# Kernel optimization log

Hardware: AMD Instinct MI355X
Metric: run time of the kernel (lower is better)

The kernel has to match this reference:

```python
import jax, jax.numpy as jnp
import numpy as np

B, N, L, E, D = 16, 16384, 192, 128, 128


def setup_inputs() -> dict:
    key = jax.random.key(0)
    ks = jax.random.split(key, 16)
    s = 0.05
    return {
        "x_L_flattened": jax.random.normal(ks[0], (B, N), jnp.float32),
        "x_y_mask_flattened": jax.random.randint(ks[1], (B, N), 0, 2).astype(jnp.float32),
        "y_mask_L_flattened": jnp.zeros((B, N), jnp.float32),
        "x_y_mark": jax.random.normal(ks[2], (B, L, 1), jnp.float32),
        "variable_indices_flattened": jax.random.randint(ks[3], (B, N), 0, E),
        "time_indices_flattened": jax.random.randint(ks[4], (B, N), 0, L),
        "N_OBSERVATIONS_MAX": N,
        # learned params (stored [in, out]; torch Linear uses x @ W.T + b)
        "W_obs": jax.random.normal(ks[5], (2, D), jnp.float32) * s,
        "b_obs": jnp.zeros((D,), jnp.float32),
        "W_time": jax.random.normal(ks[6], (1, D), jnp.float32) * s,
        "b_time": jnp.zeros((D,), jnp.float32),
        "var_hyperedge_w": jax.random.normal(ks[7], (E, D), jnp.float32),
        "W_q": jax.random.normal(ks[8], (D, D), jnp.float32) * s,
        "b_q": jnp.zeros((D,), jnp.float32),
        "W_k": jax.random.normal(ks[9], (D, D), jnp.float32) * s,
        "b_k": jnp.zeros((D,), jnp.float32),
        "W_v": jax.random.normal(ks[10], (D, D), jnp.float32) * s,
        "b_v": jnp.zeros((D,), jnp.float32),
        "threshold": jnp.float32(0.5),
        "merge_coef": jnp.float32(0.5),
    }


def reference(x_L_flattened, x_y_mask_flattened, y_mask_L_flattened, x_y_mark,
              variable_indices_flattened, time_indices_flattened, N_OBSERVATIONS_MAX,
              W_obs, b_obs, W_time, b_time, var_hyperedge_w,
              W_q, b_q, W_k, b_k, W_v, b_v, threshold, merge_coef):
    mask = x_y_mask_flattened  # [B, N]
    # node features: value + (1 - mask + y_mask) channel -> [B, N, 2]
    feats = jnp.stack([x_L_flattened, 1.0 - mask + y_mask_L_flattened], axis=-1)
    # temporal incidence: node n belongs to time-edge l iff time_idx[n] == l; [B, L, N]
    ti = (time_indices_flattened[:, None, :] == jnp.arange(L)[None, :, None]).astype(jnp.float32)
    ti = ti * mask[:, None, :]
    # variable incidence: node n belongs to var-edge e iff var_idx[n] == e; [B, E, N]
    vi = (jnp.arange(E)[None, :, None] == variable_indices_flattened[:, None, :]).astype(jnp.float32)
    vi = vi * mask[:, None, :]
    # encoders
    obs = jax.nn.relu(feats @ W_obs + b_obs) * mask[..., None]          # [B, N, D]
    temp_he = jnp.sin(x_y_mark @ W_time + b_time)                        # [B, L, D]
    var_he = jax.nn.relu(jnp.broadcast_to(var_hyperedge_w, (B, E, D)))   # [B, E, D]
    # IrregularityAwareAttention over variable hyperedges with incidence as aux
    q = var_he @ W_q + b_q
    k = var_he @ W_k + b_k
    v = var_he @ W_v + b_v
    att = jnp.einsum('bed,bfd->bef', q, k) / (D ** 0.5)                  # [B, E, E]
    att_aux = jnp.einsum('ben,bfn->bef', vi, vi) / (N_OBSERVATIONS_MAX ** 0.5)
    merge = (att > threshold) & (att_aux != 0)
    att = jnp.where(merge, (1.0 - merge_coef) * att + merge_coef * att_aux, att)
    attn = jax.nn.softmax(att, axis=-1)
    out = jnp.einsum('bef,bfd->bed', attn, v)                            # [B, E, D]
    return (obs, temp_he, out, ti, vi)
```

## Files before the change

kernel.cpp:

```cpp
#include <hip/hip_runtime.h>

#define Bb 16
#define Nn 16384
#define Ll 192
#define Ee 128
#define Dd 128


__global__ __launch_bounds__(256) void k_obs(
    const float* __restrict__ x, const float* __restrict__ mask,
    const float* __restrict__ ymask, const int* __restrict__ vidx,
    const int* __restrict__ tidx, const float* __restrict__ W_obs,
    const float* __restrict__ b_obs, float* __restrict__ obs,
    float* __restrict__ ti, float* __restrict__ vi, float* __restrict__ cnt)
{
    const int row  = (blockIdx.x << 2) + (threadIdx.x >> 6);
    const int lane = threadIdx.x & 63;
    const int b = row >> 14;
    const int n = row & (Nn - 1);

    const float m  = mask[row];
    const float xv = x[row];
    const float f1 = 1.0f - m + ymask[row];

    const int d = lane << 1;
    const float w00 = W_obs[d],      w01 = W_obs[d + 1];
    const float w10 = W_obs[Dd + d], w11 = W_obs[Dd + d + 1];
    const float bb0 = b_obs[d],      bb1 = b_obs[d + 1];

    float2 ov;
    ov.x = fmaxf(fmaf(xv, w00, fmaf(f1, w10, bb0)), 0.0f) * m;
    ov.y = fmaxf(fmaf(xv, w01, fmaf(f1, w11, bb1)), 0.0f) * m;
    *reinterpret_cast<float2*>(obs + ((size_t)row << 7) + d) = ov;

    if (lane == 0 && m != 0.0f) {
        const int t = tidx[row];
        const int e = vidx[row];
        ti[(size_t)b * (Ll * (size_t)Nn) + (size_t)t * Nn + n] = m;
        vi[((size_t)(b * Ee + e) << 14) + n] = m;
        atomicAdd(&cnt[b * Ee + e], 1.0f);
    }
}

__global__ __launch_bounds__(256) void k_temp(
    const float* __restrict__ mark, const float* __restrict__ Wt,
    const float* __restrict__ bt, float* __restrict__ temp)
{
    const int idx = blockIdx.x * 256 + threadIdx.x;
    const int d = idx & 127;
    const int r = idx >> 7;
    temp[idx] = sinf(fmaf(mark[r], Wt[d], bt[d]));
}

__global__ __launch_bounds__(128) void k_qkv(
    const float* __restrict__ var_w,
    const float* __restrict__ Wq, const float* __restrict__ bq,
    const float* __restrict__ Wk, const float* __restrict__ bk,
    const float* __restrict__ Wv, const float* __restrict__ bv,
    float* __restrict__ q, float* __restrict__ k, float* __restrict__ v)
{
    __shared__ float h[Dd];
    const int e = blockIdx.x, d = threadIdx.x;
    h[d] = fmaxf(var_w[e * Dd + d], 0.0f);
    __syncthreads();
    float aq = bq[d], ak = bk[d], av = bv[d];
    #pragma unroll 4
    for (int j = 0; j < Dd; ++j) {
        const float hj = h[j];
        aq = fmaf(hj, Wq[j * Dd + d], aq);
        ak = fmaf(hj, Wk[j * Dd + d], ak);
        av = fmaf(hj, Wv[j * Dd + d], av);
    }
    q[e * Dd + d] = aq;
    k[e * Dd + d] = ak;
    v[e * Dd + d] = av;
}

__global__ __launch_bounds__(128) void k_att0(
    const float* __restrict__ q, const float* __restrict__ k,
    float* __restrict__ att0)
{
    __shared__ float qr[Dd];
    const int e = blockIdx.x, f = threadIdx.x;
    qr[f] = q[e * Dd + f];
    __syncthreads();
    const float* kr = k + f * Dd;
    float acc = 0.0f;
    #pragma unroll 4
    for (int d = 0; d < Dd; ++d) acc = fmaf(qr[d], kr[d], acc);
    att0[e * Dd + f] = acc * 0.08838834764831845f;
}

__global__ __launch_bounds__(128) void k_soft(
    const float* __restrict__ att0, const float* __restrict__ v,
    const float* __restrict__ cnt, const float* __restrict__ thr_p,
    const float* __restrict__ mc_p, const int* __restrict__ nobs_p,
    float* __restrict__ outp)
{
    __shared__ float attn[Ee];
    __shared__ float red[4];
    const int b = blockIdx.x >> 7;
    const int e = blockIdx.x & 127;
    const int f = threadIdx.x;

    float a = att0[e * Ee + f];
    if (f == e) {
        const float c = cnt[b * Ee + e];
        const float thr = *thr_p;
        if (c != 0.0f && a > thr) {
            const float mc  = *mc_p;
            const float aux = c / sqrtf((float)(*nobs_p));
            a = (1.0f - mc) * a + mc * aux;
        }
    }
    float mx = a;
    #pragma unroll
    for (int off = 32; off > 0; off >>= 1) mx = fmaxf(mx, __shfl_xor(mx, off));
    if ((threadIdx.x & 63) == 0) red[threadIdx.x >> 6] = mx;
    __syncthreads();
    mx = fmaxf(red[0], red[1]);

    const float ex = expf(a - mx);
    float s = ex;
    #pragma unroll
    for (int off = 32; off > 0; off >>= 1) s += __shfl_xor(s, off);
    if ((threadIdx.x & 63) == 0) red[2 + (threadIdx.x >> 6)] = s;
    __syncthreads();
    s = red[2] + red[3];

    attn[f] = ex / s;
    __syncthreads();

    const int d = f;
    float acc = 0.0f;
    #pragma unroll 4
    for (int j = 0; j < Ee; ++j) acc = fmaf(attn[j], v[j * Dd + d], acc);
    outp[((size_t)(b * Ee + e) << 7) + d] = acc;
}

extern "C" void kernel_launch(void* const* d_in, const int* in_sizes, int n_in,
                              void* d_out, int out_size, void* d_ws, size_t ws_size,
                              hipStream_t stream) {
    (void)in_sizes; (void)n_in; (void)out_size; (void)ws_size;

    const float* x      = (const float*)d_in[0];
    const float* mask   = (const float*)d_in[1];
    const float* ymask  = (const float*)d_in[2];
    const float* mark   = (const float*)d_in[3];
    const int*   vidx   = (const int*)d_in[4];
    const int*   tidx   = (const int*)d_in[5];
    const int*   nobs   = (const int*)d_in[6];
    const float* W_obs  = (const float*)d_in[7];
    const float* b_obs  = (const float*)d_in[8];
    const float* W_time = (const float*)d_in[9];
    const float* b_time = (const float*)d_in[10];
    const float* var_w  = (const float*)d_in[11];
    const float* W_q    = (const float*)d_in[12];
    const float* b_q    = (const float*)d_in[13];
    const float* W_k    = (const float*)d_in[14];
    const float* b_k    = (const float*)d_in[15];
    const float* W_v    = (const float*)d_in[16];
    const float* b_v    = (const float*)d_in[17];
    const float* thr    = (const float*)d_in[18];
    const float* mc     = (const float*)d_in[19];

    float* out_base = (float*)d_out;
    float* obs  = out_base;
    float* temp = out_base + 33554432;
    float* attO = out_base + 33947648;
    float* ti   = out_base + 34209792;
    float* vi   = out_base + 84541440;

    float* ws   = (float*)d_ws;
    float* cnt  = ws;
    float* q    = ws + 2048;
    float* k    = ws + 18432;
    float* v    = ws + 34816;
    float* att0 = ws + 51200;

    hipMemsetAsync(ti, 0, (size_t)(50331648 + 33554432) * sizeof(float), stream);
    hipMemsetAsync(cnt, 0, 2048 * sizeof(float), stream);

    k_obs<<<(Bb * Nn) / 4, 256, 0, stream>>>(x, mask, ymask, vidx, tidx,
                                             W_obs, b_obs, obs, ti, vi, cnt);
    k_temp<<<(Bb * Ll * Dd) / 256, 256, 0, stream>>>(mark, W_time, b_time, temp);
    k_qkv<<<Ee, Dd, 0, stream>>>(var_w, W_q, b_q, W_k, b_k, W_v, b_v, q, k, v);
    k_att0<<<Ee, Dd, 0, stream>>>(q, k, att0);
    k_soft<<<Bb * Ee, Dd, 0, stream>>>(att0, v, cnt, thr, mc, nobs, attO);
}
```

Measured before the change: 643.5 us.

## Write dense incidence matrices directly instead of memset plus scatter

Drops the large memset of the ti/vi incidence outputs. A new kernel writes every element of both matrices with coalesced float4 stores, each thread covering four nodes, so the incidence data is written once instead of zero-filled and then scattered into. Per-variable counts are first gathered in a shared-memory histogram and then flushed to global memory with one atomic per bin. The obs kernel is split out and widened to float4 stores. The incidence kernel launches only 256 blocks, which may be too few to saturate write bandwidth.

```diff
diff --git a/kernel.cpp b/kernel.cpp
--- a/kernel.cpp
+++ b/kernel.cpp
@@ -7,39 +7,81 @@
 #define Dd 128
 
 
+__global__ __launch_bounds__(256) void k_inc(
+    const int* __restrict__ tidx, const int* __restrict__ vidx,
+    const float* __restrict__ mask,
+    float* __restrict__ ti, float* __restrict__ vi, float* __restrict__ cnt)
+{
+    __shared__ float hcnt[Ee];
+    const int tid = threadIdx.x;
+    if (tid < Ee) hcnt[tid] = 0.0f;
+    __syncthreads();
+
+    const int g  = blockIdx.x * 256 + tid;
+    const int b  = g >> 12;
+    const int n4 = (g & 4095) << 2;
+
+    const int4   t4 = *reinterpret_cast<const int4*>(tidx + b * Nn + n4);
+    const int4   v4 = *reinterpret_cast<const int4*>(vidx + b * Nn + n4);
+    const float4 m4 = *reinterpret_cast<const float4*>(mask + b * Nn + n4);
+
+    if (m4.x != 0.0f) atomicAdd(&hcnt[v4.x], 1.0f);
+    if (m4.y != 0.0f) atomicAdd(&hcnt[v4.y], 1.0f);
+    if (m4.z != 0.0f) atomicAdd(&hcnt[v4.z], 1.0f);
+    if (m4.w != 0.0f) atomicAdd(&hcnt[v4.w], 1.0f);
+
+    float* tib = ti + (((size_t)b * Ll) << 14) + n4;
+    #pragma unroll 4
+    for (int l = 0; l < Ll; ++l) {
+        float4 o;
+        o.x = (t4.x == l) ? m4.x : 0.0f;
+        o.y = (t4.y == l) ? m4.y : 0.0f;
+        o.z = (t4.z == l) ? m4.z : 0.0f;
+        o.w = (t4.w == l) ? m4.w : 0.0f;
+        *reinterpret_cast<float4*>(tib + ((size_t)l << 14)) = o;
+    }
+
+    float* vib = vi + (((size_t)b * Ee) << 14) + n4;
+    #pragma unroll 4
+    for (int e = 0; e < Ee; ++e) {
+        float4 o;
+        o.x = (v4.x == e) ? m4.x : 0.0f;
+        o.y = (v4.y == e) ? m4.y : 0.0f;
+        o.z = (v4.z == e) ? m4.z : 0.0f;
+        o.w = (v4.w == e) ? m4.w : 0.0f;
+        *reinterpret_cast<float4*>(vib + ((size_t)e << 14)) = o;
+    }
+
+    __syncthreads();
+    if (tid < Ee) {
+        const float c = hcnt[tid];
+        if (c != 0.0f) atomicAdd(&cnt[b * Ee + tid], c);
+    }
+}
+
 __global__ __launch_bounds__(256) void k_obs(
     const float* __restrict__ x, const float* __restrict__ mask,
-    const float* __restrict__ ymask, const int* __restrict__ vidx,
-    const int* __restrict__ tidx, const float* __restrict__ W_obs,
-    const float* __restrict__ b_obs, float* __restrict__ obs,
-    float* __restrict__ ti, float* __restrict__ vi, float* __restrict__ cnt)
-{
-    const int row  = (blockIdx.x << 2) + (threadIdx.x >> 6);
-    const int lane = threadIdx.x & 63;
-    const int b = row >> 14;
-    const int n = row & (Nn - 1);
+    const float* __restrict__ ymask, const float* __restrict__ W_obs,
+    const float* __restrict__ b_obs, float* __restrict__ obs)
+{
+    const int g   = blockIdx.x * 256 + threadIdx.x;
+    const int row = g >> 5;
+    const int d   = (g & 31) << 2;
 
     const float m  = mask[row];
     const float xv = x[row];
     const float f1 = 1.0f - m + ymask[row];
 
-    const int d = lane << 1;
-    const float w00 = W_obs[d],      w01 = W_obs[d + 1];
-    const float w10 = W_obs[Dd + d], w11 = W_obs[Dd + d + 1];
-    const float bb0 = b_obs[d],      bb1 = b_obs[d + 1];
-
-    float2 ov;
-    ov.x = fmaxf(fmaf(xv, w00, fmaf(f1, w10, bb0)), 0.0f) * m;
-    ov.y = fmaxf(fmaf(xv, w01, fmaf(f1, w11, bb1)), 0.0f) * m;
-    *reinterpret_cast<float2*>(obs + ((size_t)row << 7) + d) = ov;
-
-    if (lane == 0 && m != 0.0f) {
-        const int t = tidx[row];
-        const int e = vidx[row];
-        ti[(size_t)b * (Ll * (size_t)Nn) + (size_t)t * Nn + n] = m;
-        vi[((size_t)(b * Ee + e) << 14) + n] = m;
-        atomicAdd(&cnt[b * Ee + e], 1.0f);
-    }
+    const float4 w0 = *reinterpret_cast<const float4*>(W_obs + d);
+    const float4 w1 = *reinterpret_cast<const float4*>(W_obs + Dd + d);
+    const float4 bb = *reinterpret_cast<const float4*>(b_obs + d);
+
+    float4 o;
+    o.x = fmaxf(fmaf(xv, w0.x, fmaf(f1, w1.x, bb.x)), 0.0f) * m;
+    o.y = fmaxf(fmaf(xv, w0.y, fmaf(f1, w1.y, bb.y)), 0.0f) * m;
+    o.z = fmaxf(fmaf(xv, w0.z, fmaf(f1, w1.z, bb.z)), 0.0f) * m;
+    o.w = fmaxf(fmaf(xv, w0.w, fmaf(f1, w1.w, bb.w)), 0.0f) * m;
+    *reinterpret_cast<float4*>(obs + ((size_t)row << 7) + d) = o;
 }
 
 __global__ __launch_bounds__(256) void k_temp(
@@ -178,11 +220,10 @@
     float* v    = ws + 34816;
     float* att0 = ws + 51200;
 
-    hipMemsetAsync(ti, 0, (size_t)(50331648 + 33554432) * sizeof(float), stream);
     hipMemsetAsync(cnt, 0, 2048 * sizeof(float), stream);
 
-    k_obs<<<(Bb * Nn) / 4, 256, 0, stream>>>(x, mask, ymask, vidx, tidx,
-                                             W_obs, b_obs, obs, ti, vi, cnt);
+    k_inc<<<(Bb * Nn) / (4 * 256), 256, 0, stream>>>(tidx, vidx, mask, ti, vi, cnt);
+    k_obs<<<(Bb * Nn * 32) / 256, 256, 0, stream>>>(x, mask, ymask, W_obs, b_obs, obs);
     k_temp<<<(Bb * Ll * Dd) / 256, 256, 0, stream>>>(mark, W_time, b_time, temp);
     k_qkv<<<Ee, Dd, 0, stream>>>(var_w, W_q, b_q, W_k, b_k, W_v, b_v, q, k, v);
     k_att0<<<Ee, Dd, 0, stream>>>(q, k, att0);
```

New measurement: 591.0 us. 8.2% less time.
